# Performance work log

Measured on AMD Instinct MI355X. Metric: run time of the kernel, lower is better.

The kernel has to match this reference:

```python
import jax, jax.numpy as jnp
import numpy as np

NUM_HEADS = 16
EPS = 1e-12  # matches F.normalize eps


def _l2norm(x):
    return x / jnp.maximum(jnp.linalg.norm(x, axis=-1, keepdims=True), EPS)


def setup_inputs() -> dict:
    key = jax.random.key(0)
    ks = jax.random.split(key, 8)
    B, S, E, M = 2, 2048, 1024, 16384
    sc = 0.02
    return {
        "hidden_states": jax.random.normal(ks[0], (B, S, E), jnp.float32),
        "memory_keys": jax.random.normal(ks[1], (M, E), jnp.float32),
        "memory_values": jax.random.normal(ks[2], (M, E), jnp.float32),
        "Wq": jax.random.normal(ks[3], (E, E), jnp.float32) * sc,
        "bq": jnp.zeros((E,), jnp.float32),
        "Wk": jax.random.normal(ks[4], (E, E), jnp.float32) * sc,
        "bk": jnp.zeros((E,), jnp.float32),
        "Wv": jax.random.normal(ks[5], (E, E), jnp.float32) * sc,
        "bv": jnp.zeros((E,), jnp.float32),
        "Wo": jax.random.normal(ks[6], (E, E), jnp.float32) * sc,
        "bo": jnp.zeros((E,), jnp.float32),
        "top_k": 8,
    }


def reference(hidden_states, memory_keys, memory_values, Wq, bq, Wk, bk, Wv, bv, Wo, bo, top_k):
    B, S, E = hidden_states.shape
    H = NUM_HEADS
    hd = E // H
    scale = 1.0 / jnp.sqrt(jnp.float32(hd))

    def heads(x):  # [B,S,E] -> [B,H,S,hd]
        return x.reshape(B, S, H, hd).transpose(0, 2, 1, 3)

    q = heads(hidden_states @ Wq.T + bq)
    k = heads(hidden_states @ Wk.T + bk)
    v = heads(hidden_states @ Wv.T + bv)

    # self-attention scores [B,H,S,S]
    scores = jnp.einsum('bhqd,bhkd->bhqk', q, k) * scale

    # memory retrieval: cosine sim of raw hidden states vs memory keys
    qn = _l2norm(hidden_states)           # [B,S,E]
    kn = _l2norm(memory_keys)             # [M,E]
    sims = jnp.einsum('bse,me->bsm', qn, kn)   # [B,S,M]
    top_vals, top_idx = jax.lax.top_k(sims, top_k)  # [B,S,K]
    retrieved = memory_values[top_idx]    # [B,S,K,E] gather
    ret_h = retrieved.reshape(B, S, top_k, H, hd).transpose(0, 3, 1, 2, 4)  # [B,H,S,K,hd]

    # concat retrieval similarities as extra attention columns, re-softmax
    mem_scores = jnp.broadcast_to(top_vals[:, None, :, :], (B, H, S, top_k))
    ext = jnp.concatenate([scores, mem_scores], axis=-1)   # [B,H,S,S+K]
    probs = jax.nn.softmax(ext, axis=-1)

    ctx = jnp.einsum('bhqk,bhkd->bhqd', probs[..., :S], v)
    ctx = ctx + jnp.einsum('bhqk,bhqkd->bhqd', probs[..., S:], ret_h)

    ctx = ctx.transpose(0, 2, 1, 3).reshape(B, S, E)
    return ctx @ Wo.T + bo
```

## Files before the change

### kernel.cpp

```cpp
#include <hip/hip_runtime.h>
#include <math.h>

#define R_TOT 4096
#define E_DIM 1024
#define M_DIM 16384
#define H_NUM 16
#define HD    64
#define SEQ   2048
#define BATCH 2
#define TOPK  8
#define MIDK  16
#define NCHUNK 16
#define SCHUNK 1024
#define CANDS  32

typedef __attribute__((ext_vector_type(8))) short short8_t;
typedef __attribute__((ext_vector_type(4))) float f32x4;

__device__ inline unsigned short f2bf(float x) {
  unsigned u = __float_as_uint(x);
  u = (u + 0x7fff + ((u >> 16) & 1)) >> 16;
  return (unsigned short)u;
}
__device__ inline float bf2f(unsigned short h) {
  return __uint_as_float(((unsigned)h) << 16);
}

#define GLDS16(gp, lp) __builtin_amdgcn_global_load_lds( \
    (const __attribute__((address_space(1))) void*)(gp), \
    (__attribute__((address_space(3))) void*)(lp), 16, 0, 0)

__global__ __launch_bounds__(256) void norm_bf16_kernel(const float* __restrict__ X,
                                                        unsigned short* __restrict__ Y,
                                                        unsigned short* __restrict__ Yraw,
                                                        float* __restrict__ rinv_out) {
  int row = blockIdx.x;
  int tid = threadIdx.x;
  const float4* xr = (const float4*)(X + (size_t)row * E_DIM);
  float4 v = xr[tid];
  float s = v.x*v.x + v.y*v.y + v.z*v.z + v.w*v.w;
  #pragma unroll
  for (int off = 32; off; off >>= 1) s += __shfl_down(s, off, 64);
  __shared__ float wsum[4];
  if ((tid & 63) == 0) wsum[tid >> 6] = s;
  __syncthreads();
  float tot = wsum[0] + wsum[1] + wsum[2] + wsum[3];
  float rinv = 1.0f / fmaxf(sqrtf(tot), 1e-12f);
  if (tid == 0) rinv_out[row] = rinv;
  ushort4 o;
  o.x = f2bf(v.x * rinv); o.y = f2bf(v.y * rinv);
  o.z = f2bf(v.z * rinv); o.w = f2bf(v.w * rinv);
  ((ushort4*)(Y + (size_t)row * E_DIM))[tid] = o;
  if (Yraw) {
    ushort4 o2;
    o2.x = f2bf(v.x); o2.y = f2bf(v.y); o2.z = f2bf(v.z); o2.w = f2bf(v.w);
    ((ushort4*)(Yraw + (size_t)row * E_DIM))[tid] = o2;
  }
}

__global__ __launch_bounds__(256) void cast_bf16_kernel(const float* __restrict__ X,
                                                        unsigned short* __restrict__ Y, int n4) {
  int i = blockIdx.x * 256 + threadIdx.x;
  if (i < n4) {
    float4 v = ((const float4*)X)[i];
    ushort4 o;
    o.x = f2bf(v.x); o.y = f2bf(v.y); o.z = f2bf(v.z); o.w = f2bf(v.w);
    ((ushort4*)Y)[i] = o;
  }
}

template<int OUT_BF16>
__device__ __forceinline__ void gemm_tile_body(
    const unsigned short* __restrict__ Ab, const unsigned short* __restrict__ Bb,
    const float* __restrict__ bias, void* __restrict__ C, int N,
    int bm, int bn, char* pool) {
  short* Ap = (short*)pool;
  short* Bp = (short*)(pool + 16384);
  int tid = threadIdx.x;
  int wave = tid >> 6, lane = tid & 63;
  int wr = wave >> 1, wc = wave & 1;
  int li8 = lane >> 3;
  int gslot = (lane & 7) ^ li8;

  f32x4 acc[4][4];
  #pragma unroll
  for (int i = 0; i < 4; ++i)
    #pragma unroll
    for (int j = 0; j < 4; ++j)
      acc[i][j] = (f32x4){0.f, 0.f, 0.f, 0.f};

  for (int k0 = 0; k0 < E_DIM; k0 += 64) {
    #pragma unroll
    for (int s4 = 0; s4 < 8; ++s4) {
      int s = wave * 8 + s4;
      const unsigned short* gp;
      if (s < 16) {
        int r = s * 8 + li8;
        gp = Ab + (size_t)(bm + r) * E_DIM + k0 + gslot * 8;
      } else {
        int r = (s - 16) * 8 + li8;
        gp = Bb + (size_t)(bn + r) * E_DIM + k0 + gslot * 8;
      }
      GLDS16(gp, pool + s * 1024);
    }
    __syncthreads();
    #pragma unroll
    for (int ks = 0; ks < 2; ++ks) {
      short8_t af[4], bf[4];
      int kslot = ks * 4 + (lane >> 4);
      #pragma unroll
      for (int mi = 0; mi < 4; ++mi) {
        int r = wr * 64 + mi * 16 + (lane & 15);
        af[mi] = *(const short8_t*)(Ap + r * 64 + ((kslot ^ (r & 7)) * 8));
      }
      #pragma unroll
      for (int ni = 0; ni < 4; ++ni) {
        int r = wc * 64 + ni * 16 + (lane & 15);
        bf[ni] = *(const short8_t*)(Bp + r * 64 + ((kslot ^ (r & 7)) * 8));
      }
      #pragma unroll
      for (int mi = 0; mi < 4; ++mi)
        #pragma unroll
        for (int ni = 0; ni < 4; ++ni)
          acc[mi][ni] = __builtin_amdgcn_mfma_f32_16x16x32_bf16(af[mi], bf[ni], acc[mi][ni], 0, 0, 0);
    }
    __syncthreads();
  }
  #pragma unroll
  for (int mi = 0; mi < 4; ++mi) {
    #pragma unroll
    for (int ni = 0; ni < 4; ++ni) {
      int col = bn + wc * 64 + ni * 16 + (lane & 15);
      float bv = bias[col];
      #pragma unroll
      for (int r = 0; r < 4; ++r) {
        int row = bm + wr * 64 + mi * 16 + (lane >> 4) * 4 + r;
        float v = acc[mi][ni][r] + bv;
        if (OUT_BF16)
          ((unsigned short*)C)[(size_t)row * N + col] = f2bf(v);
        else
          ((float*)C)[(size_t)row * N + col] = v;
      }
    }
  }
}

__global__ __launch_bounds__(256) void mfma_gemm_out(
    const unsigned short* __restrict__ Ab, const unsigned short* __restrict__ Bb,
    const float* __restrict__ bias, float* __restrict__ C) {
  __shared__ __align__(16) char pool[32768];
  gemm_tile_body<0>(Ab, Bb, bias, C, E_DIM, blockIdx.x * 128, blockIdx.y * 128, pool);
}

__global__ __launch_bounds__(256) void mfma_gemm_qkv(
    const unsigned short* __restrict__ hb,
    const unsigned short* __restrict__ wq, const unsigned short* __restrict__ wk,
    const unsigned short* __restrict__ wv,
    const float* __restrict__ bq, const float* __restrict__ bk, const float* __restrict__ bv,
    unsigned short* __restrict__ q_b, unsigned short* __restrict__ k_b,
    unsigned short* __restrict__ v_b) {
  __shared__ __align__(16) char pool[32768];
  int bn_g = blockIdx.y * 128;
  int sel = bn_g >> 10;
  int bn = bn_g & 1023;
  const unsigned short* Bb = (sel == 0) ? wq : (sel == 1) ? wk : wv;
  const float* bias = (sel == 0) ? bq : (sel == 1) ? bk : bv;
  unsigned short* C = (sel == 0) ? q_b : (sel == 1) ? k_b : v_b;
  gemm_tile_body<1>(hb, Bb, bias, C, E_DIM, blockIdx.x * 128, bn, pool);
}

__global__ __launch_bounds__(256) void vtrans_kernel(const unsigned short* __restrict__ vb,
                                                     unsigned short* __restrict__ vT) {
  int st = blockIdx.x;
  int bh = blockIdx.y;
  int b = bh >> 4, h = bh & 15;
  __shared__ short T[64][72];
  int tid = threadIdx.x;
  #pragma unroll
  for (int it = 0; it < 2; ++it) {
    int idx = tid + it * 256;
    int r = idx >> 3, sl = idx & 7;
    short8_t v = *(const short8_t*)(vb + ((size_t)(b * SEQ + st * 64 + r)) * E_DIM + h * HD + sl * 8);
    *(short8_t*)&T[r][sl * 8] = v;
  }
  __syncthreads();
  int d = tid >> 2, sp = (tid & 3) * 16;
  short8_t o0, o1;
  #pragma unroll
  for (int u = 0; u < 8; ++u) o0[u] = T[sp + u][d];
  #pragma unroll
  for (int u = 0; u < 8; ++u) o1[u] = T[sp + 8 + u][d];
  size_t base = ((size_t)bh * HD + d) * SEQ + st * 64 + sp;
  *(short8_t*)(vT + base) = o0;
  *(short8_t*)(vT + base + 8) = o1;
}

#define SPITCH 132
#define NSTEP (SCHUNK / 128 * 16)

__global__ __launch_bounds__(512) void sims_topk_kernel(
    const unsigned short* __restrict__ Hn, const unsigned short* __restrict__ MKn,
    float* __restrict__ cand_v, int* __restrict__ cand_i) {
  __shared__ __align__(16) char pool[98304 + 128 * SPITCH * 2];
  short* Sp = (short*)(pool + 98304);

  int f = blockIdx.x + blockIdx.y * gridDim.x;
  int xs = f & 7, js = f >> 3;
  int bm = (js & 31) * 128;
  int chunk = xs + 8 * (js >> 5);

  int tid = threadIdx.x;
  int wave = tid >> 6, lane = tid & 63;
  int wr = wave >> 2, wc = wave & 3;
  int srow = tid >> 2, sl = tid & 3;
  int li8 = lane >> 3;
  int gslot = (lane & 7) ^ li8;

  float tv[TOPK]; int ti[TOPK];
  #pragma unroll
  for (int u = 0; u < TOPK; ++u) { tv[u] = -INFINITY; ti[u] = 0; }

  auto STAGE = [&](int d, int t) {
    int sub = t >> 4;
    int k0 = (t & 15) * 64;
    int bn = chunk * SCHUNK + sub * 128;
    #pragma unroll
    for (int s4 = 0; s4 < 4; ++s4) {
      int s = wave * 4 + s4;
      const unsigned short* gp;
      if (s < 16) {
        int r = s * 8 + li8;
        gp = Hn + (size_t)(bm + r) * E_DIM + k0 + gslot * 8;
      } else {
        int r = (s - 16) * 8 + li8;
        gp = MKn + (size_t)(bn + r) * E_DIM + k0 + gslot * 8;
      }
      GLDS16(gp, pool + d * 32768 + s * 1024);
    }
  };

  f32x4 acc[4][2];
  #pragma unroll
  for (int i = 0; i < 4; ++i)
    #pragma unroll
    for (int j = 0; j < 2; ++j)
      acc[i][j] = (f32x4){0.f, 0.f, 0.f, 0.f};

  STAGE(0, 0);
  STAGE(1, 1);

  for (int t = 0; t < NSTEP; ++t) {
    int cur = t % 3;
    if (t + 2 < NSTEP) {
      STAGE((t + 2) % 3, t + 2);
      asm volatile("s_waitcnt vmcnt(8)" ::: "memory");
    } else if (t + 1 < NSTEP) {
      asm volatile("s_waitcnt vmcnt(4)" ::: "memory");
    } else {
      asm volatile("s_waitcnt vmcnt(0)" ::: "memory");
    }
    __builtin_amdgcn_s_barrier();
    __builtin_amdgcn_sched_barrier(0);

    short* Ap = (short*)(pool + cur * 32768);
    short* Bp = (short*)(pool + cur * 32768 + 16384);
    #pragma unroll
    for (int ks = 0; ks < 2; ++ks) {
      short8_t af[4], bf[2];
      int kslot = ks * 4 + (lane >> 4);
      #pragma unroll
      for (int mi = 0; mi < 4; ++mi) {
        int r = wr * 64 + mi * 16 + (lane & 15);
        af[mi] = *(const short8_t*)(Ap + r * 64 + ((kslot ^ (r & 7)) * 8));
      }
      #pragma unroll
      for (int ni = 0; ni < 2; ++ni) {
        int r = wc * 32 + ni * 16 + (lane & 15);
        bf[ni] = *(const short8_t*)(Bp + r * 64 + ((kslot ^ (r & 7)) * 8));
      }
      #pragma unroll
      for (int mi = 0; mi < 4; ++mi)
        #pragma unroll
        for (int ni = 0; ni < 2; ++ni)
          acc[mi][ni] = __builtin_amdgcn_mfma_f32_16x16x32_bf16(af[mi], bf[ni], acc[mi][ni], 0, 0, 0);
    }
    __builtin_amdgcn_sched_barrier(0);
    __builtin_amdgcn_s_barrier();

    if ((t & 15) == 15) {
      int bn = chunk * SCHUNK + (t >> 4) * 128;
      #pragma unroll
      for (int mi = 0; mi < 4; ++mi) {
        #pragma unroll
        for (int ni = 0; ni < 2; ++ni) {
          int scol = wc * 32 + ni * 16 + (lane & 15);
          #pragma unroll
          for (int r = 0; r < 4; ++r) {
            int srw = wr * 64 + mi * 16 + (lane >> 4) * 4 + r;
            Sp[srw * SPITCH + scol] = (short)f2bf(acc[mi][ni][r]);
          }
          acc[mi][ni] = (f32x4){0.f, 0.f, 0.f, 0.f};
        }
      }
      __syncthreads();
      #pragma unroll
      for (int u4 = 0; u4 < 8; ++u4) {
        const short* p = Sp + srow * SPITCH + sl * 32 + u4 * 4;
        short4 v4 = *(const short4*)p;
        short vv[4] = {v4.x, v4.y, v4.z, v4.w};
        #pragma unroll
        for (int j = 0; j < 4; ++j) {
          float v = bf2f((unsigned short)vv[j]);
          if (v > tv[0]) {
            int idx = bn + sl * 32 + u4 * 4 + j;
            int p_ = 0;
            #pragma unroll
            for (int q = 1; q < TOPK; ++q)
              if (v > tv[q]) { tv[q-1] = tv[q]; ti[q-1] = ti[q]; p_ = q; }
            tv[p_] = v; ti[p_] = idx;
          }
        }
      }
      __syncthreads();
    }
  }
  size_t base = (((size_t)(bm + srow)) * NCHUNK + chunk) * CANDS + sl * TOPK;
  #pragma unroll
  for (int u = 0; u < TOPK; ++u) { cand_v[base + u] = tv[u]; cand_i[base + u] = ti[u]; }
}

__global__ __launch_bounds__(64) void merge_topk_kernel(
    const float* __restrict__ cand_v, const int* __restrict__ cand_i,
    int* __restrict__ mid_i) {
  int row = blockIdx.x;
  int lane = threadIdx.x;
  size_t base = (size_t)row * (NCHUNK * CANDS);
  float v[8]; int id[8];
  #pragma unroll
  for (int u = 0; u < 8; ++u) {
    v[u]  = cand_v[base + lane*8 + u];
    id[u] = cand_i[base + lane*8 + u];
  }
  for (int t = 0; t < MIDK; ++t) {
    float bvv = v[0]; int bu = 0;
    #pragma unroll
    for (int u = 1; u < 8; ++u) if (v[u] > bvv) { bvv = v[u]; bu = u; }
    float mv = bvv; int ml = lane;
    #pragma unroll
    for (int off = 32; off; off >>= 1) {
      float ov = __shfl_down(mv, off, 64);
      int   ol = __shfl_down(ml, off, 64);
      if (ov > mv) { mv = ov; ml = ol; }
    }
    ml = __shfl(ml, 0, 64);
    if (lane == ml) {
      mid_i[(size_t)row * MIDK + t] = id[bu];
      v[bu] = -INFINITY;
    }
  }
}

__global__ __launch_bounds__(256) void refine_kernel(
    const float* __restrict__ hidden, const float* __restrict__ mkeys,
    const float* __restrict__ rinvH, const float* __restrict__ rinvK,
    const int* __restrict__ mid_i,
    float* __restrict__ top_v, int* __restrict__ top_i) {
  int row = blockIdx.x;
  int tid = threadIdx.x;
  int wave = tid >> 6, lane = tid & 63;
  __shared__ float hrow[E_DIM];
  __shared__ float rv[MIDK];
  __shared__ int   ri[MIDK];
  ((float4*)hrow)[tid] = ((const float4*)(hidden + (size_t)row * E_DIM))[tid];
  __syncthreads();
  float rh = rinvH[row];
  for (int c = wave; c < MIDK; c += 4) {
    int idx = mid_i[(size_t)row * MIDK + c];
    const float* kp = mkeys + (size_t)idx * E_DIM;
    float s = 0.f;
    #pragma unroll
    for (int rr = 0; rr < 4; ++rr) {
      float4 kv = *(const float4*)(kp + rr * 256 + lane * 4);
      float4 hv = *(const float4*)(hrow + rr * 256 + lane * 4);
      s += hv.x*kv.x + hv.y*kv.y + hv.z*kv.z + hv.w*kv.w;
    }
    #pragma unroll
    for (int off = 32; off; off >>= 1) s += __shfl_down(s, off, 64);
    if (lane == 0) { rv[c] = s * rh * rinvK[idx]; ri[c] = idx; }
  }
  __syncthreads();
  if (tid == 0) {
    bool used[MIDK] = {};
    #pragma unroll
    for (int t = 0; t < TOPK; ++t) {
      float best = -INFINITY; int bi = -1; int bidx = 0x7fffffff;
      for (int c = 0; c < MIDK; ++c) {
        if (used[c]) continue;
        if (rv[c] > best || (rv[c] == best && ri[c] < bidx)) {
          best = rv[c]; bi = c; bidx = ri[c];
        }
      }
      used[bi] = true;
      top_v[(size_t)row * TOPK + t] = best;
      top_i[(size_t)row * TOPK + t] = bidx;
    }
  }
}

__global__ __launch_bounds__(256) void flash_mfma_kernel(
    const unsigned short* __restrict__ qb, const unsigned short* __restrict__ kb,
    const unsigned short* __restrict__ vT, const float* __restrict__ MV,
    const float* __restrict__ top_v, const int* __restrict__ top_i,
    unsigned short* __restrict__ ctx) {
  __shared__ __align__(16) char pool[32768];
  short* Kp = (short*)pool;
  short* Vp = (short*)(pool + 8192);
  int qt = blockIdx.x;
  int bh = blockIdx.y;
  int b = bh >> 4, h = bh & 15;
  int tid = threadIdx.x;
  int wave = tid >> 6, lane = tid & 63;
  int g = lane >> 4, c = lane & 15;
  int li8 = lane >> 3;
  int gslot = (lane & 7) ^ li8;
  short* Pw = (short*)(pool + 16384 + wave * 4096);
  const float scale = 0.125f;

  short8_t aQ[2][2];
  #pragma unroll
  for (int mi = 0; mi < 2; ++mi)
    #pragma unroll
    for (int ks = 0; ks < 2; ++ks) {
      size_t row = (size_t)b * SEQ + qt * 128 + wave * 32 + mi * 16 + c;
      aQ[mi][ks] = *(const short8_t*)(qb + row * E_DIM + h * HD + (ks * 4 + g) * 8);
    }

  f32x4 oa[2][4];
  #pragma unroll
  for (int mi = 0; mi < 2; ++mi)
    #pragma unroll
    for (int nd = 0; nd < 4; ++nd)
      oa[mi][nd] = (f32x4){0.f, 0.f, 0.f, 0.f};
  float m_[2][4], l_[2][4];
  #pragma unroll
  for (int mi = 0; mi < 2; ++mi)
    #pragma unroll
    for (int r = 0; r < 4; ++r) { m_[mi][r] = -INFINITY; l_[mi][r] = 0.f; }

  for (int kv0 = 0; kv0 < SEQ; kv0 += 64) {
    #pragma unroll
    for (int j = 0; j < 4; ++j) {
      int s = wave * 4 + j;
      const unsigned short* gp;
      if (s < 8) {
        int r = s * 8 + li8;
        gp = kb + ((size_t)(b * SEQ + kv0 + r)) * E_DIM + h * HD + gslot * 8;
      } else {
        int d = (s - 8) * 8 + li8;
        gp = vT + ((size_t)(bh * HD + d)) * SEQ + kv0 + gslot * 8;
      }
      GLDS16(gp, pool + s * 1024);
    }
    __syncthreads();

    f32x4 sa[2][4];
    #pragma unroll
    for (int mi = 0; mi < 2; ++mi)
      #pragma unroll
      for (int ni = 0; ni < 4; ++ni)
        sa[mi][ni] = (f32x4){0.f, 0.f, 0.f, 0.f};
    #pragma unroll
    for (int ks = 0; ks < 2; ++ks) {
      short8_t bK[4];
      #pragma unroll
      for (int ni = 0; ni < 4; ++ni) {
        int r = ni * 16 + c;
        bK[ni] = *(const short8_t*)(Kp + r * 64 + (((ks * 4 + g) ^ (r & 7)) * 8));
      }
      #pragma unroll
      for (int mi = 0; mi < 2; ++mi)
        #pragma unroll
        for (int ni = 0; ni < 4; ++ni)
          sa[mi][ni] = __builtin_amdgcn_mfma_f32_16x16x32_bf16(aQ[mi][ks], bK[ni], sa[mi][ni], 0, 0, 0);
    }
    #pragma unroll
    for (int mi = 0; mi < 2; ++mi)
      #pragma unroll
      for (int ni = 0; ni < 4; ++ni)
        #pragma unroll
        for (int r = 0; r < 4; ++r)
          sa[mi][ni][r] *= scale;
    float fsc[2][4];
    #pragma unroll
    for (int mi = 0; mi < 2; ++mi)
      #pragma unroll
      for (int r = 0; r < 4; ++r) {
        float m0 = fmaxf(fmaxf(sa[mi][0][r], sa[mi][1][r]), fmaxf(sa[mi][2][r], sa[mi][3][r]));
        #pragma unroll
        for (int off = 1; off < 16; off <<= 1) m0 = fmaxf(m0, __shfl_xor(m0, off, 64));
        float mn = fmaxf(m_[mi][r], m0);
        fsc[mi][r] = __expf(m_[mi][r] - mn);
        m_[mi][r] = mn;
      }
    #pragma unroll
    for (int mi = 0; mi < 2; ++mi)
      #pragma unroll
      for (int nd = 0; nd < 4; ++nd)
        #pragma unroll
        for (int r = 0; r < 4; ++r)
          oa[mi][nd][r] *= fsc[mi][r];
    #pragma unroll
    for (int mi = 0; mi < 2; ++mi)
      #pragma unroll
      for (int r = 0; r < 4; ++r) {
        float ps = 0.f;
        #pragma unroll
        for (int ni = 0; ni < 4; ++ni) {
          float p = __expf(sa[mi][ni][r] - m_[mi][r]);
          sa[mi][ni][r] = p;
          ps += p;
        }
        #pragma unroll
        for (int off = 1; off < 16; off <<= 1) ps += __shfl_xor(ps, off, 64);
        l_[mi][r] = l_[mi][r] * fsc[mi][r] + ps;
      }
    #pragma unroll
    for (int mi = 0; mi < 2; ++mi)
      #pragma unroll
      for (int ni = 0; ni < 4; ++ni)
        #pragma unroll
        for (int r = 0; r < 4; ++r) {
          int ql = mi * 16 + g * 4 + r;
          int slot = (ni * 2 + (c >> 3)) ^ (ql & 7);
          Pw[ql * 64 + slot * 8 + (c & 7)] = (short)f2bf(sa[mi][ni][r]);
        }
    #pragma unroll
    for (int ks = 0; ks < 2; ++ks) {
      short8_t aP[2], bV[4];
      #pragma unroll
      for (int mi = 0; mi < 2; ++mi) {
        int ql = mi * 16 + c;
        aP[mi] = *(const short8_t*)(Pw + ql * 64 + (((ks * 4 + g) ^ (ql & 7)) * 8));
      }
      #pragma unroll
      for (int nd = 0; nd < 4; ++nd) {
        int dr = nd * 16 + c;
        bV[nd] = *(const short8_t*)(Vp + dr * 64 + (((ks * 4 + g) ^ (dr & 7)) * 8));
      }
      #pragma unroll
      for (int mi = 0; mi < 2; ++mi)
        #pragma unroll
        for (int nd = 0; nd < 4; ++nd)
          oa[mi][nd] = __builtin_amdgcn_mfma_f32_16x16x32_bf16(aP[mi], bV[nd], oa[mi][nd], 0, 0, 0);
    }
    __syncthreads();
  }

  #pragma unroll
  for (int mi = 0; mi < 2; ++mi)
    #pragma unroll
    for (int r = 0; r < 4; ++r) {
      size_t row = (size_t)b * SEQ + qt * 128 + wave * 32 + mi * 16 + g * 4 + r;
      const float* tvp = top_v + row * TOPK;
      const int*   tip = top_i + row * TOPK;
      float lg[TOPK];
      float mmax = m_[mi][r];
      #pragma unroll
      for (int j = 0; j < TOPK; ++j) { lg[j] = tvp[j]; mmax = fmaxf(mmax, lg[j]); }
      float f = __expf(m_[mi][r] - mmax);
      float l = l_[mi][r] * f;
      #pragma unroll
      for (int nd = 0; nd < 4; ++nd) oa[mi][nd][r] *= f;
      #pragma unroll
      for (int j = 0; j < TOPK; ++j) {
        float p = __expf(lg[j] - mmax);
        l += p;
        const float* mvp = MV + (size_t)tip[j] * E_DIM + h * HD + c;
        #pragma unroll
        for (int nd = 0; nd < 4; ++nd)
          oa[mi][nd][r] = fmaf(p, mvp[nd * 16], oa[mi][nd][r]);
      }
      float inv = 1.0f / l;
      #pragma unroll
      for (int nd = 0; nd < 4; ++nd)
        ctx[row * E_DIM + h * HD + nd * 16 + c] = f2bf(oa[mi][nd][r] * inv);
    }
}

extern "C" void kernel_launch(void* const* d_in, const int* in_sizes, int n_in,
                              void* d_out, int out_size, void* d_ws, size_t ws_size,
                              hipStream_t stream) {
  (void)in_sizes; (void)n_in; (void)out_size; (void)ws_size;
  const float* hidden = (const float*)d_in[0];
  const float* mkeys  = (const float*)d_in[1];
  const float* mvals  = (const float*)d_in[2];
  const float* Wq = (const float*)d_in[3];
  const float* bq = (const float*)d_in[4];
  const float* Wk = (const float*)d_in[5];
  const float* bk = (const float*)d_in[6];
  const float* Wv = (const float*)d_in[7];
  const float* bv = (const float*)d_in[8];
  const float* Wo = (const float*)d_in[9];
  const float* bo = (const float*)d_in[10];

  char* ws = (char*)d_ws;
  float* cand_v = (float*)ws;                                  ws += (size_t)R_TOT * NCHUNK * CANDS * 4;
  int*   cand_i = (int*)ws;                                    ws += (size_t)R_TOT * NCHUNK * CANDS * 4;
  int*   mid_i  = (int*)ws;                                    ws += (size_t)R_TOT * MIDK * 4;
  float* top_v  = (float*)ws;                                  ws += (size_t)R_TOT * TOPK * 4;
  int*   top_i  = (int*)ws;                                    ws += (size_t)R_TOT * TOPK * 4;
  float* rinvH  = (float*)ws;                                  ws += (size_t)R_TOT * 4;
  float* rinvK  = (float*)ws;                                  ws += (size_t)M_DIM * 4;
  unsigned short* Hn   = (unsigned short*)ws;                  ws += (size_t)R_TOT * E_DIM * 2;
  unsigned short* MKn  = (unsigned short*)ws;                  ws += (size_t)M_DIM * E_DIM * 2;
  unsigned short* hb   = (unsigned short*)ws;                  ws += (size_t)R_TOT * E_DIM * 2;
  unsigned short* wqb  = (unsigned short*)ws;                  ws += (size_t)E_DIM * E_DIM * 2;
  unsigned short* wkb  = (unsigned short*)ws;                  ws += (size_t)E_DIM * E_DIM * 2;
  unsigned short* wvb  = (unsigned short*)ws;                  ws += (size_t)E_DIM * E_DIM * 2;
  unsigned short* wob  = (unsigned short*)ws;                  ws += (size_t)E_DIM * E_DIM * 2;
  unsigned short* q_b  = (unsigned short*)ws;                  ws += (size_t)R_TOT * E_DIM * 2;
  unsigned short* k_b  = (unsigned short*)ws;                  ws += (size_t)R_TOT * E_DIM * 2;
  unsigned short* v_b  = (unsigned short*)ws;                  ws += (size_t)R_TOT * E_DIM * 2;
  unsigned short* vTb  = (unsigned short*)ws;                  ws += (size_t)R_TOT * E_DIM * 2;
  unsigned short* ctxb = (unsigned short*)ws;                  ws += (size_t)R_TOT * E_DIM * 2;

  norm_bf16_kernel<<<dim3(R_TOT), 256, 0, stream>>>(hidden, Hn, hb, rinvH);
  norm_bf16_kernel<<<dim3(M_DIM), 256, 0, stream>>>(mkeys, MKn, (unsigned short*)nullptr, rinvK);

  int n4w = E_DIM * E_DIM / 4;
  cast_bf16_kernel<<<dim3(n4w / 256), 256, 0, stream>>>(Wq, wqb, n4w);
  cast_bf16_kernel<<<dim3(n4w / 256), 256, 0, stream>>>(Wk, wkb, n4w);
  cast_bf16_kernel<<<dim3(n4w / 256), 256, 0, stream>>>(Wv, wvb, n4w);
  cast_bf16_kernel<<<dim3(n4w / 256), 256, 0, stream>>>(Wo, wob, n4w);

  mfma_gemm_qkv<<<dim3(R_TOT / 128, 3 * E_DIM / 128), 256, 0, stream>>>(
      hb, wqb, wkb, wvb, bq, bk, bv, q_b, k_b, v_b);

  vtrans_kernel<<<dim3(SEQ / 64, BATCH * H_NUM), 256, 0, stream>>>(v_b, vTb);

  sims_topk_kernel<<<dim3(R_TOT / 128, NCHUNK), 512, 0, stream>>>(Hn, MKn, cand_v, cand_i);
  merge_topk_kernel<<<dim3(R_TOT), 64, 0, stream>>>(cand_v, cand_i, mid_i);
  refine_kernel<<<dim3(R_TOT), 256, 0, stream>>>(hidden, mkeys, rinvH, rinvK, mid_i, top_v, top_i);

  flash_mfma_kernel<<<dim3(SEQ / 128, BATCH * H_NUM), 256, 0, stream>>>(
      q_b, k_b, vTb, mvals, top_v, top_i, ctxb);

  mfma_gemm_out<<<dim3(R_TOT / 128, E_DIM / 128), 256, 0, stream>>>(ctxb, wob, bo, (float*)d_out);
}
```

Baseline: 585.7 us.

## Double-buffer LDS tiles in GEMM and flash attention kernels with async prefetch

The GEMM tile body and the flash attention kernel now use two LDS buffers. The next K-slice or KV tile is issued via global-to-LDS loads before computing on the current one, with explicit vmcnt waits and raw barriers in place of __syncthreads. Flash attention also stages Q through LDS with a swizzled layout instead of loading it directly from global memory. LDS per block doubles, which can lower occupancy. The sims_topk block-index remapping is reverted to a plain grid mapping, which may lose the cache locality the remap provided.

```diff
diff --git a/kernel.cpp b/kernel.cpp
--- a/kernel.cpp
+++ b/kernel.cpp
@@ -70,26 +70,17 @@
 }
 
 template<int OUT_BF16>
-__device__ __forceinline__ void gemm_tile_body(
+__device__ __forceinline__ void gemm_tile_body_pipe(
     const unsigned short* __restrict__ Ab, const unsigned short* __restrict__ Bb,
     const float* __restrict__ bias, void* __restrict__ C, int N,
     int bm, int bn, char* pool) {
-  short* Ap = (short*)pool;
-  short* Bp = (short*)(pool + 16384);
   int tid = threadIdx.x;
   int wave = tid >> 6, lane = tid & 63;
   int wr = wave >> 1, wc = wave & 1;
   int li8 = lane >> 3;
   int gslot = (lane & 7) ^ li8;
 
-  f32x4 acc[4][4];
-  #pragma unroll
-  for (int i = 0; i < 4; ++i)
-    #pragma unroll
-    for (int j = 0; j < 4; ++j)
-      acc[i][j] = (f32x4){0.f, 0.f, 0.f, 0.f};
-
-  for (int k0 = 0; k0 < E_DIM; k0 += 64) {
+  auto STAGE = [&](int d, int k0) {
     #pragma unroll
     for (int s4 = 0; s4 < 8; ++s4) {
       int s = wave * 8 + s4;
@@ -101,9 +92,31 @@
         int r = (s - 16) * 8 + li8;
         gp = Bb + (size_t)(bn + r) * E_DIM + k0 + gslot * 8;
       }
-      GLDS16(gp, pool + s * 1024);
-    }
-    __syncthreads();
+      GLDS16(gp, pool + d * 32768 + s * 1024);
+    }
+  };
+
+  f32x4 acc[4][4];
+  #pragma unroll
+  for (int i = 0; i < 4; ++i)
+    #pragma unroll
+    for (int j = 0; j < 4; ++j)
+      acc[i][j] = (f32x4){0.f, 0.f, 0.f, 0.f};
+
+  STAGE(0, 0);
+
+  for (int t = 0; t < E_DIM / 64; ++t) {
+    int cur = t & 1;
+    if (t + 1 < E_DIM / 64) {
+      STAGE(1 - cur, (t + 1) * 64);
+      asm volatile("s_waitcnt vmcnt(8)" ::: "memory");
+    } else {
+      asm volatile("s_waitcnt vmcnt(0)" ::: "memory");
+    }
+    __builtin_amdgcn_s_barrier();
+    __builtin_amdgcn_sched_barrier(0);
+    short* Ap = (short*)(pool + cur * 32768);
+    short* Bp = (short*)(pool + cur * 32768 + 16384);
     #pragma unroll
     for (int ks = 0; ks < 2; ++ks) {
       short8_t af[4], bf[4];
@@ -124,7 +137,8 @@
         for (int ni = 0; ni < 4; ++ni)
           acc[mi][ni] = __builtin_amdgcn_mfma_f32_16x16x32_bf16(af[mi], bf[ni], acc[mi][ni], 0, 0, 0);
     }
-    __syncthreads();
+    __builtin_amdgcn_sched_barrier(0);
+    __builtin_amdgcn_s_barrier();
   }
   #pragma unroll
   for (int mi = 0; mi < 4; ++mi) {
@@ -148,8 +162,8 @@
 __global__ __launch_bounds__(256) void mfma_gemm_out(
     const unsigned short* __restrict__ Ab, const unsigned short* __restrict__ Bb,
     const float* __restrict__ bias, float* __restrict__ C) {
-  __shared__ __align__(16) char pool[32768];
-  gemm_tile_body<0>(Ab, Bb, bias, C, E_DIM, blockIdx.x * 128, blockIdx.y * 128, pool);
+  __shared__ __align__(16) char pool[65536];
+  gemm_tile_body_pipe<0>(Ab, Bb, bias, C, E_DIM, blockIdx.x * 128, blockIdx.y * 128, pool);
 }
 
 __global__ __launch_bounds__(256) void mfma_gemm_qkv(
@@ -159,14 +173,14 @@
     const float* __restrict__ bq, const float* __restrict__ bk, const float* __restrict__ bv,
     unsigned short* __restrict__ q_b, unsigned short* __restrict__ k_b,
     unsigned short* __restrict__ v_b) {
-  __shared__ __align__(16) char pool[32768];
+  __shared__ __align__(16) char pool[65536];
   int bn_g = blockIdx.y * 128;
   int sel = bn_g >> 10;
   int bn = bn_g & 1023;
   const unsigned short* Bb = (sel == 0) ? wq : (sel == 1) ? wk : wv;
   const float* bias = (sel == 0) ? bq : (sel == 1) ? bk : bv;
   unsigned short* C = (sel == 0) ? q_b : (sel == 1) ? k_b : v_b;
-  gemm_tile_body<1>(hb, Bb, bias, C, E_DIM, blockIdx.x * 128, bn, pool);
+  gemm_tile_body_pipe<1>(hb, Bb, bias, C, E_DIM, blockIdx.x * 128, bn, pool);
 }
 
 __global__ __launch_bounds__(256) void vtrans_kernel(const unsigned short* __restrict__ vb,
@@ -204,10 +218,8 @@
   __shared__ __align__(16) char pool[98304 + 128 * SPITCH * 2];
   short* Sp = (short*)(pool + 98304);
 
-  int f = blockIdx.x + blockIdx.y * gridDim.x;
-  int xs = f & 7, js = f >> 3;
-  int bm = (js & 31) * 128;
-  int chunk = xs + 8 * (js >> 5);
+  int bm = blockIdx.x * 128;
+  int chunk = blockIdx.y;
 
   int tid = threadIdx.x;
   int wave = tid >> 6, lane = tid & 63;
@@ -412,9 +424,8 @@
     const unsigned short* __restrict__ vT, const float* __restrict__ MV,
     const float* __restrict__ top_v, const int* __restrict__ top_i,
     unsigned short* __restrict__ ctx) {
-  __shared__ __align__(16) char pool[32768];
-  short* Kp = (short*)pool;
-  short* Vp = (short*)(pool + 8192);
+  __shared__ __align__(16) char pool[65536];
+  short* Qs = (short*)pool;
   int qt = blockIdx.x;
   int bh = blockIdx.y;
   int b = bh >> 4, h = bh & 15;
@@ -423,31 +434,10 @@
   int g = lane >> 4, c = lane & 15;
   int li8 = lane >> 3;
   int gslot = (lane & 7) ^ li8;
-  short* Pw = (short*)(pool + 16384 + wave * 4096);
+  short* Pw = (short*)(pool + 49152 + wave * 4096);
   const float scale = 0.125f;
 
-  short8_t aQ[2][2];
-  #pragma unroll
-  for (int mi = 0; mi < 2; ++mi)
-    #pragma unroll
-    for (int ks = 0; ks < 2; ++ks) {
-      size_t row = (size_t)b * SEQ + qt * 128 + wave * 32 + mi * 16 + c;
-      aQ[mi][ks] = *(const short8_t*)(qb + row * E_DIM + h * HD + (ks * 4 + g) * 8);
-    }
-
-  f32x4 oa[2][4];
-  #pragma unroll
-  for (int mi = 0; mi < 2; ++mi)
-    #pragma unroll
-    for (int nd = 0; nd < 4; ++nd)
-      oa[mi][nd] = (f32x4){0.f, 0.f, 0.f, 0.f};
-  float m_[2][4], l_[2][4];
-  #pragma unroll
-  for (int mi = 0; mi < 2; ++mi)
-    #pragma unroll
-    for (int r = 0; r < 4; ++r) { m_[mi][r] = -INFINITY; l_[mi][r] = 0.f; }
-
-  for (int kv0 = 0; kv0 < SEQ; kv0 += 64) {
+  auto STAGEKV = [&](int d, int kv0) {
     #pragma unroll
     for (int j = 0; j < 4; ++j) {
       int s = wave * 4 + j;
@@ -456,12 +446,57 @@
         int r = s * 8 + li8;
         gp = kb + ((size_t)(b * SEQ + kv0 + r)) * E_DIM + h * HD + gslot * 8;
       } else {
-        int d = (s - 8) * 8 + li8;
-        gp = vT + ((size_t)(bh * HD + d)) * SEQ + kv0 + gslot * 8;
-      }
-      GLDS16(gp, pool + s * 1024);
-    }
-    __syncthreads();
+        int dd = (s - 8) * 8 + li8;
+        gp = vT + ((size_t)(bh * HD + dd)) * SEQ + kv0 + gslot * 8;
+      }
+      GLDS16(gp, pool + 16384 + d * 16384 + s * 1024);
+    }
+  };
+
+  #pragma unroll
+  for (int j = 0; j < 4; ++j) {
+    int s = wave * 4 + j;
+    int r = s * 8 + li8;
+    const unsigned short* gp = qb + ((size_t)(b * SEQ) + qt * 128 + r) * E_DIM + h * HD + gslot * 8;
+    GLDS16(gp, pool + s * 1024);
+  }
+  STAGEKV(0, 0);
+  __syncthreads();
+
+  short8_t aQ[2][2];
+  #pragma unroll
+  for (int mi = 0; mi < 2; ++mi)
+    #pragma unroll
+    for (int ks = 0; ks < 2; ++ks) {
+      int r = wave * 32 + mi * 16 + c;
+      int slot = ks * 4 + g;
+      aQ[mi][ks] = *(const short8_t*)(Qs + r * 64 + ((slot ^ (r & 7)) * 8));
+    }
+
+  f32x4 oa[2][4];
+  #pragma unroll
+  for (int mi = 0; mi < 2; ++mi)
+    #pragma unroll
+    for (int nd = 0; nd < 4; ++nd)
+      oa[mi][nd] = (f32x4){0.f, 0.f, 0.f, 0.f};
+  float m_[2][4], l_[2][4];
+  #pragma unroll
+  for (int mi = 0; mi < 2; ++mi)
+    #pragma unroll
+    for (int r = 0; r < 4; ++r) { m_[mi][r] = -INFINITY; l_[mi][r] = 0.f; }
+
+  for (int kt = 0; kt < SEQ / 64; ++kt) {
+    int cur = kt & 1;
+    if (kt + 1 < SEQ / 64) {
+      STAGEKV(1 - cur, (kt + 1) * 64);
+      asm volatile("s_waitcnt vmcnt(4)" ::: "memory");
+    } else {
+      asm volatile("s_waitcnt vmcnt(0)" ::: "memory");
+    }
+    __builtin_amdgcn_s_barrier();
+    __builtin_amdgcn_sched_barrier(0);
+    short* Kp = (short*)(pool + 16384 + cur * 16384);
+    short* Vp = (short*)(pool + 16384 + cur * 16384 + 8192);
 
     f32x4 sa[2][4];
     #pragma unroll
@@ -553,7 +588,8 @@
         for (int nd = 0; nd < 4; ++nd)
           oa[mi][nd] = __builtin_amdgcn_mfma_f32_16x16x32_bf16(aP[mi], bV[nd], oa[mi][nd], 0, 0, 0);
     }
-    __syncthreads();
+    __builtin_amdgcn_sched_barrier(0);
+    __builtin_amdgcn_s_barrier();
   }
 
   #pragma unroll
```

Measured after the change: 570.5 us. -2.6%, faster.
